# Optimization experiments

Hardware: AMD Instinct MI355X
Metric: run time of the kernel (lower is better)

The kernel has to match this reference:

```python
import jax, jax.numpy as jnp
import numpy as np

DIN = 1024
DOUT = 1024


def setup_inputs() -> dict:
    key = jax.random.key(0)
    kx, kq, kk, kv = jax.random.split(key, 4)
    B, T = 4, 2048
    x = jax.random.normal(kx, (B, T, DIN), dtype=jnp.float32)
    # nn.Linear weights are (dout, din); init like PyTorch default scale
    s = 1.0 / np.sqrt(DIN)
    Wq = jax.random.uniform(kq, (DOUT, DIN), minval=-s, maxval=s, dtype=jnp.float32)
    Wk = jax.random.uniform(kk, (DOUT, DIN), minval=-s, maxval=s, dtype=jnp.float32)
    Wv = jax.random.uniform(kv, (DOUT, DIN), minval=-s, maxval=s, dtype=jnp.float32)
    return {"x": x, "Wq": Wq, "Wk": Wk, "Wv": Wv}


def reference(x, Wq, Wk, Wv):
    B, T, _ = x.shape
    q = jnp.einsum('btd,ed->bte', x, Wq)
    k = jnp.einsum('btd,ed->bte', x, Wk)
    v = jnp.einsum('btd,ed->bte', x, Wv)
    attn = jnp.einsum('bqe,bke->bqk', q, k)  # [B, T, T]
    # Faithful to source: masked_fill result is discarded, so the causal mask
    # is a MULTIPLICATIVE tril of ones (upper triangle logits become 0, not -inf).
    mask = jnp.tril(jnp.ones((T, T), dtype=attn.dtype))
    attn = attn * mask
    # Faithful to source: scale by sqrt(last dim of attn) = sqrt(T), not sqrt(d).
    attn = jax.nn.softmax(attn / jnp.sqrt(jnp.asarray(T, attn.dtype)), axis=-1)
    return jnp.einsum('bqk,bke->bqe', attn, v)
```

## Files before the change

### kernel.cpp

```cpp
#include <hip/hip_runtime.h>
#include <stdint.h>

#define BB 4
#define TT 2048
#define DD 1024
#define NX (BB*TT*DD)
#define NW (DD*DD)
#define SCALE 0.022097086912079608f
#define SCALEI 2.157918643757774e-5f
#define UNSCALE 7.689469810104304e-6f
#define Q8F 2.4606299212598425e-4f
#define VQ 48.0f
#define PVF (1.0f/3072.0f)
#define TQF (1.0f/24.0f)

typedef short v8s __attribute__((ext_vector_type(8)));
typedef float v4f __attribute__((ext_vector_type(4)));
typedef int   v4i __attribute__((ext_vector_type(4)));
typedef uint8_t u8;

typedef const void __attribute__((address_space(1))) *as1_cvp;
typedef void __attribute__((address_space(3))) *as3_vp;

__device__ __forceinline__ short f2bf(float f) {
    union { float f; uint32_t u; } x; x.f = f;
    uint32_t r = x.u + 0x7fffu + ((x.u >> 16) & 1u);
    return (short)(r >> 16);
}

__device__ __forceinline__ void gl_lds16(const void* g, const void* lds_wave_base) {
    __builtin_amdgcn_global_load_lds(
        (as1_cvp)(uintptr_t)g,
        (as3_vp)(uint32_t)(uintptr_t)lds_wave_base,
        16, 0, 0);
}

#define WAITV(N) asm volatile("s_waitcnt vmcnt(" #N ")" ::: "memory")

__device__ __forceinline__ void stage128B(const u8* __restrict__ g, int lda,
                                          u8* lds, int tid) {
    #pragma unroll
    for (int s = 0; s < 2; s++) {
        int t = s * 512 + tid;
        int r = t >> 3, c = t & 7, cg = c ^ (r & 7);
        gl_lds16(g + (size_t)r * lda + cg * 16, lds + s * 8192 + (tid >> 6) * 1024);
    }
}
__device__ __forceinline__ void stB8(const u8* __restrict__ g, u8* lds, int tid, int p) {
    #pragma unroll
    for (int s = 0; s < 2; s++) {
        int t = s * 512 + tid;
        int r = t >> 3, c = t & 7, cg = c ^ (r & 7);
        int grow = ((r >> 5) << 6) + p * 32 + (r & 31);
        gl_lds16(g + (size_t)grow * 1024 + cg * 16, lds + s * 8192 + (tid >> 6) * 1024);
    }
}
__device__ __forceinline__ v4i frag16(const u8* lds, int row, int c) {
    return *(const v4i*)(lds + row * 128 + ((c ^ (row & 7)) << 4));
}

__device__ __forceinline__ void stage64(const u8* __restrict__ g, u8* lds, int tid) {
    int r = tid >> 2, c = tid & 3;
    gl_lds16(g + (size_t)r * 1024 + c * 16, lds + (tid >> 6) * 1024);
}
__device__ __forceinline__ v4i fragK64(const u8* lds, int row, int gq) {
    return *(const v4i*)(lds + row * 64 + gq * 16);
}

__global__ void k_convert(const float* __restrict__ x, const float* __restrict__ Wq,
                          const float* __restrict__ Wk, const float* __restrict__ Wv,
                          u8* __restrict__ dst8, float* __restrict__ rowsum,
                          float* __restrict__ TSpart, int* __restrict__ TQint) {
    int i = blockIdx.x * 256 + threadIdx.x;
    if (i < BB * TT) rowsum[i] = (float)((15 - ((i & 2047) >> 7)) * 128);
    if (i < BB * 16 * 1024) { TSpart[i] = 0.f; TQint[i] = 0; }
    size_t base = (size_t)i * 4;
    const float* src; size_t off; float sc; bool clip;
    if (base < NX)               { src = x;  off = base; sc = 32.f; clip = true; }
    else if (base < NX + NW)     { src = Wq; off = base - NX; sc = 4064.f; clip = false; }
    else if (base < NX + 2*(size_t)NW) { src = Wk; off = base - NX - NW; sc = 4064.f; clip = false; }
    else                         { src = Wv; off = base - NX - 2*(size_t)NW; sc = 4064.f; clip = false; }
    float4 f = *(const float4*)(src + off);
    float a0 = f.x * sc, a1 = f.y * sc, a2 = f.z * sc, a3 = f.w * sc;
    if (clip) {
        a0 = fminf(fmaxf(a0, -127.f), 127.f);
        a1 = fminf(fmaxf(a1, -127.f), 127.f);
        a2 = fminf(fmaxf(a2, -127.f), 127.f);
        a3 = fminf(fmaxf(a3, -127.f), 127.f);
    }
    int q0 = __float2int_rn(a0), q1 = __float2int_rn(a1);
    int q2 = __float2int_rn(a2), q3 = __float2int_rn(a3);
    uint32_t w = (uint32_t)(q0 & 255) | ((uint32_t)(q1 & 255) << 8) |
                 ((uint32_t)(q2 & 255) << 16) | ((uint32_t)(q3 & 255) << 24);
    *(uint32_t*)(dst8 + base) = w;
}

__global__ __launch_bounds__(512, 2) void k_qkv(const u8* __restrict__ xb,
                                                const u8* __restrict__ wb,
                                                u8* __restrict__ q8,
                                                u8* __restrict__ k8,
                                                u8* __restrict__ vt8,
                                                float* __restrict__ TSpart,
                                                int* __restrict__ TQint) {
    int h = blockIdx.x;
    int w = (h & 7) * 96 + (h >> 3);
    int which = w >> 8, rem = w & 255, ntile = rem >> 6, mtile = rem & 63;
    int m0 = mtile * 128, n0 = ntile * 256;
    const u8* Ag = xb + (size_t)m0 * 1024;
    const u8* Bg = wb + (size_t)which * NW + (size_t)n0 * 1024;
    __shared__ __align__(16) u8 SH[98304];
    int tid = threadIdx.x, lane = tid & 63, wave = tid >> 6;
    int wm = wave >> 2, wn = wave & 3;
    int lr = lane & 15, lq = lane >> 4;
    int arow = wm * 64 + lr;
    int brow = wn * 32 + lr;
    v4i acc[4][4];
    #pragma unroll
    for (int i = 0; i < 4; i++)
        #pragma unroll
        for (int j = 0; j < 4; j++) acc[i][j] = (v4i){0, 0, 0, 0};

    stage128B(Ag, 1024, SH, tid);
    stB8(Bg, SH + 16384, tid, 0);
    stB8(Bg, SH + 32768, tid, 1);

    #pragma unroll
    for (int t = 0; t < 8; ++t) {
        u8* S  = SH + (t & 1) * 49152;
        u8* Sn = SH + ((t + 1) & 1) * 49152;
        const u8* Agn = Ag + (t + 1) * 128;
        const u8* Bgn = Bg + (t + 1) * 128;
        WAITV(2);
        __builtin_amdgcn_s_barrier();
        v4i af[4][2], bf[2][2];
        #pragma unroll
        for (int i = 0; i < 4; i++)
            #pragma unroll
            for (int kh = 0; kh < 2; kh++) af[i][kh] = frag16(S, arow + i * 16, kh * 4 + lq);
        #pragma unroll
        for (int jj = 0; jj < 2; jj++)
            #pragma unroll
            for (int kh = 0; kh < 2; kh++) bf[jj][kh] = frag16(S + 16384, brow + jj * 16, kh * 4 + lq);
        if (t < 7) {
            stage128B(Agn, 1024, Sn,  tid);
            stB8(Bgn, Sn + 16384, tid, 0);
        }
        __builtin_amdgcn_s_setprio(1);
        #pragma unroll
        for (int kh = 0; kh < 2; kh++)
            #pragma unroll
            for (int i = 0; i < 4; i++)
                #pragma unroll
                for (int jj = 0; jj < 2; jj++)
                    acc[i][jj] = __builtin_amdgcn_mfma_i32_16x16x64_i8(af[i][kh], bf[jj][kh], acc[i][jj], 0, 0, 0);
        __builtin_amdgcn_s_setprio(0);
        if (t < 7) { WAITV(4); }
        else       { WAITV(0); }
        __builtin_amdgcn_s_barrier();
        v4i bg2[2][2];
        #pragma unroll
        for (int jj = 0; jj < 2; jj++)
            #pragma unroll
            for (int kh = 0; kh < 2; kh++) bg2[jj][kh] = frag16(S + 32768, brow + jj * 16, kh * 4 + lq);
        if (t < 7) stB8(Bgn, Sn + 32768, tid, 1);
        __builtin_amdgcn_s_setprio(1);
        #pragma unroll
        for (int kh = 0; kh < 2; kh++)
            #pragma unroll
            for (int i = 0; i < 4; i++)
                #pragma unroll
                for (int jj = 0; jj < 2; jj++)
                    acc[i][2 + jj] = __builtin_amdgcn_mfma_i32_16x16x64_i8(af[i][kh], bg2[jj][kh], acc[i][2 + jj], 0, 0, 0);
        __builtin_amdgcn_s_setprio(0);
    }

    if (which == 2) {
        int bb = m0 >> 11, jt = (m0 & 2047) >> 7;
        #pragma unroll
        for (int bI = 0; bI < 4; bI++) {
            int col = n0 + wn * 64 + bI * 16 + lr;
            float sf = 0.f; int si = 0;
            #pragma unroll
            for (int a = 0; a < 4; a++) {
                int row0 = m0 + wm * 64 + a * 16 + lq * 4;
                int tt0 = row0 & 2047;
                size_t idx = ((size_t)bb << 21) + ((size_t)col << 11) + tt0;
                float v0 = (float)acc[a][bI][0] * UNSCALE;
                float v1 = (float)acc[a][bI][1] * UNSCALE;
                float v2 = (float)acc[a][bI][2] * UNSCALE;
                float v3 = (float)acc[a][bI][3] * UNSCALE;
                sf += v0 + v1 + v2 + v3;
                int c0 = __float2int_rn(fminf(fmaxf(v0 * VQ, -127.f), 127.f));
                int c1 = __float2int_rn(fminf(fmaxf(v1 * VQ, -127.f), 127.f));
                int c2 = __float2int_rn(fminf(fmaxf(v2 * VQ, -127.f), 127.f));
                int c3 = __float2int_rn(fminf(fmaxf(v3 * VQ, -127.f), 127.f));
                si += c0 + c1 + c2 + c3;
                uint32_t pw = (uint32_t)(c0 & 255) | ((uint32_t)(c1 & 255) << 8) |
                              ((uint32_t)(c2 & 255) << 16) | ((uint32_t)(c3 & 255) << 24);
                *(uint32_t*)(vt8 + idx) = pw;
            }
            sf += __shfl_xor(sf, 16); sf += __shfl_xor(sf, 32);
            si += __shfl_xor(si, 16); si += __shfl_xor(si, 32);
            if (lq == 0) {
                atomicAdd(&TSpart[(size_t)(bb * 16 + jt) * 1024 + col], sf);
                atomicAdd(&TQint[(size_t)(bb * 16 + jt) * 1024 + col], si);
            }
        }
    } else {
        u8* outp = (which == 0) ? q8 : k8;
        #pragma unroll
        for (int a = 0; a < 4; a++)
            #pragma unroll
            for (int b = 0; b < 4; b++)
                #pragma unroll
                for (int r = 0; r < 4; r++) {
                    int row = m0 + wm * 64 + a * 16 + lq * 4 + r;
                    int col = n0 + wn * 64 + b * 16 + lr;
                    float v = (float)acc[a][b][r] * Q8F;
                    v = fminf(fmaxf(v, -127.f), 127.f);
                    outp[(size_t)row * 1024 + col] = (u8)(__float2int_rn(v) & 255);
                }
    }
}

__global__ __launch_bounds__(512, 4) void k_pk(const u8* __restrict__ q8,
                                               const u8* __restrict__ k8,
                                               char* __restrict__ P8,
                                               float* __restrict__ rowsum) {
    int pidx = blockIdx.x, b = blockIdx.z;
    int qt = 0;
    while ((qt + 1) * (qt + 2) / 2 <= pidx) qt++;
    int kt = pidx - qt * (qt + 1) / 2;
    int r0 = qt * 128;
    const u8* Ag = q8 + ((size_t)b * 2048 + r0) * 1024;
    const u8* Bg = k8 + ((size_t)b * 2048 + (size_t)kt * 128) * 1024;
    __shared__ __align__(16) u8 SH[49152];
    int tid = threadIdx.x, lane = tid & 63, wave = tid >> 6;
    int wm2 = wave >> 2, wn4 = wave & 3;
    int lr = lane & 15, lq = lane >> 4;
    v4i acc[4][2];
    #pragma unroll
    for (int i = 0; i < 4; i++)
        #pragma unroll
        for (int j = 0; j < 2; j++) acc[i][j] = (v4i){0, 0, 0, 0};

    stage64(Ag,      SH,                tid);
    stage64(Bg,      SH + 8192,         tid);
    stage64(Ag + 64, SH + 16384,        tid);
    stage64(Bg + 64, SH + 16384 + 8192, tid);

    #pragma unroll
    for (int it = 0; it < 16; ++it) {
        if (it + 1 < 16) { WAITV(2); }
        else             { WAITV(0); }
        __builtin_amdgcn_s_barrier();
        if (it + 2 < 16) {
            u8* Sn = SH + ((it + 2) % 3) * 16384;
            stage64(Ag + (it + 2) * 64, Sn,        tid);
            stage64(Bg + (it + 2) * 64, Sn + 8192, tid);
        }
        const u8* S = SH + (it % 3) * 16384;
        v4i af[4], bf[2];
        #pragma unroll
        for (int i = 0; i < 4; i++) af[i] = fragK64(S, wm2 * 64 + i * 16 + lr, lq);
        #pragma unroll
        for (int j = 0; j < 2; j++) bf[j] = fragK64(S + 8192, wn4 * 32 + j * 16 + lr, lq);
        __builtin_amdgcn_s_setprio(1);
        #pragma unroll
        for (int i = 0; i < 4; i++)
            #pragma unroll
            for (int j = 0; j < 2; j++)
                acc[i][j] = __builtin_amdgcn_mfma_i32_16x16x64_i8(af[i], bf[j], acc[i][j], 0, 0, 0);
        __builtin_amdgcn_s_setprio(0);
    }
    char* Pb = P8 + ((size_t)b << 22);
    float rs[4][4];
    #pragma unroll
    for (int i = 0; i < 4; i++)
        #pragma unroll
        for (int r = 0; r < 4; r++) rs[i][r] = 0.f;
    #pragma unroll
    for (int i = 0; i < 4; i++)
        #pragma unroll
        for (int j = 0; j < 2; j++)
            #pragma unroll
            for (int r = 0; r < 4; r++) {
                int qi = r0 + wm2 * 64 + i * 16 + lq * 4 + r;
                int kj = kt * 128 + wn4 * 32 + j * 16 + lr;
                float p = (kj <= qi) ? __expf((float)acc[i][j][r] * SCALEI) : 1.0f;
                int u = __float2int_rn(fminf(p * 64.f, 255.f));
                Pb[(size_t)qi * 2048 + kj] = (char)(u - 128);
                rs[i][r] += (float)u * 0.015625f;
            }
    #pragma unroll
    for (int m = 1; m < 16; m <<= 1)
        #pragma unroll
        for (int i = 0; i < 4; i++)
            #pragma unroll
            for (int r = 0; r < 4; r++) rs[i][r] += __shfl_xor(rs[i][r], m);
    if (lr == 0)
        #pragma unroll
        for (int i = 0; i < 4; i++)
            #pragma unroll
            for (int r = 0; r < 4; r++)
                atomicAdd(&rowsum[b * 2048 + r0 + wm2 * 64 + i * 16 + lq * 4 + r], rs[i][r]);
}

__global__ __launch_bounds__(512, 2) void k_pv(const u8* __restrict__ P8,
                                               const u8* __restrict__ vt8,
                                               const float* __restrict__ rowsum,
                                               const float* __restrict__ TSpart,
                                               const int* __restrict__ TQint,
                                               float* __restrict__ out) {
    int et = blockIdx.x, p = blockIdx.y, b = blockIdx.z;
    const u8* Bg = vt8 + ((size_t)b << 21) + (size_t)et * 128 * 2048;
    __shared__ __align__(16) u8 SH[98304];
    __shared__ float tsq[128], tqq[128];
    int tid = threadIdx.x, lane = tid & 63, wave = tid >> 6;
    int wm2 = wave >> 2, wn4 = wave & 3;
    int lr = lane & 15, lq = lane >> 4;

    #pragma unroll
    for (int ph = 0; ph < 2; ph++) {
        int qt = ph ? p : 15 - p;
        int r0 = qt * 128;
        int iters = qt + 1;
        const u8* Ag = P8 + ((size_t)b << 22) + (size_t)r0 * 2048;
        v4i acc[4][2];
        #pragma unroll
        for (int i = 0; i < 4; i++)
            #pragma unroll
            for (int j = 0; j < 2; j++) acc[i][j] = (v4i){0, 0, 0, 0};

        stage128B(Ag, 2048, SH,         tid);
        stage128B(Bg, 2048, SH + 16384, tid);
        if (iters > 1) {
            stage128B(Ag + 128, 2048, SH + 32768,         tid);
            stage128B(Bg + 128, 2048, SH + 32768 + 16384, tid);
        }
        if (tid < 128) {
            int e = et * 128 + tid;
            float ts = 0.f;
            for (int jt = qt + 1; jt < 16; jt++) ts += TSpart[(size_t)(b * 16 + jt) * 1024 + e];
            int tq = 0;
            for (int jt = 0; jt <= qt; jt++) tq += TQint[(size_t)(b * 16 + jt) * 1024 + e];
            tsq[tid] = ts;
            tqq[tid] = (float)tq;
            asm volatile("s_waitcnt lgkmcnt(0)" ::: "memory");
        }

        for (int it = 0; it < iters; ++it) {
            if (it + 1 < iters) { WAITV(4); }
            else                { WAITV(0); }
            __builtin_amdgcn_s_barrier();
            if (it + 2 < iters) {
                u8* Sn = SH + ((it + 2) % 3) * 32768;
                stage128B(Ag + (it + 2) * 128, 2048, Sn,         tid);
                stage128B(Bg + (it + 2) * 128, 2048, Sn + 16384, tid);
            }
            const u8* S = SH + (it % 3) * 32768;
            v4i af[4][2], bf[2][2];
            #pragma unroll
            for (int i = 0; i < 4; i++)
                #pragma unroll
                for (int kh = 0; kh < 2; kh++) af[i][kh] = frag16(S, wm2 * 64 + i * 16 + lr, kh * 4 + lq);
            #pragma unroll
            for (int j = 0; j < 2; j++)
                #pragma unroll
                for (int kh = 0; kh < 2; kh++) bf[j][kh] = frag16(S + 16384, wn4 * 32 + j * 16 + lr, kh * 4 + lq);
            __builtin_amdgcn_s_setprio(1);
            #pragma unroll
            for (int kh = 0; kh < 2; kh++)
                #pragma unroll
                for (int i = 0; i < 4; i++)
                    #pragma unroll
                    for (int j = 0; j < 2; j++)
                        acc[i][j] = __builtin_amdgcn_mfma_i32_16x16x64_i8(af[i][kh], bf[j][kh], acc[i][j], 0, 0, 0);
            __builtin_amdgcn_s_setprio(0);
        }
        #pragma unroll
        for (int i = 0; i < 4; i++)
            #pragma unroll
            for (int j = 0; j < 2; j++)
                #pragma unroll
                for (int r = 0; r < 4; r++) {
                    int row = r0 + wm2 * 64 + i * 16 + lq * 4 + r;
                    int cl = wn4 * 32 + j * 16 + lr;
                    int col = et * 128 + cl;
                    float numer = (float)acc[i][j][r] * PVF + tqq[cl] * TQF + tsq[cl];
                    out[((size_t)(b * 2048 + row) << 10) + col] = numer / rowsum[b * 2048 + row];
                }
        __builtin_amdgcn_s_barrier();
    }
}

extern "C" void kernel_launch(void* const* d_in, const int* in_sizes, int n_in,
                              void* d_out, int out_size, void* d_ws, size_t ws_size,
                              hipStream_t stream) {
    const float* x  = (const float*)d_in[0];
    const float* Wq = (const float*)d_in[1];
    const float* Wk = (const float*)d_in[2];
    const float* Wv = (const float*)d_in[3];
    float* out = (float*)d_out;
    char* ws = (char*)d_ws;

    u8*    xb8    = (u8*)(ws + 0);
    u8*    q8     = (u8*)(ws + 11534336);
    u8*    k8     = (u8*)(ws + 19922944);
    u8*    vt8    = (u8*)(ws + 28311552);
    char*  P8     = (char*)(ws + 36700160);
    float* rowsum = (float*)(ws + 53477376);
    float* TSpart = (float*)(ws + 53510144);
    int*   TQint  = (int*)(ws + 53772288);

    k_convert<<<11264, 256, 0, stream>>>(x, Wq, Wk, Wv, xb8, rowsum, TSpart, TQint);
    k_qkv<<<dim3(768, 1, 1), 512, 0, stream>>>(xb8, xb8 + NX, q8, k8, vt8, TSpart, TQint);
    k_pk<<<dim3(136, 1, 4), 512, 0, stream>>>(q8, k8, P8, rowsum);
    k_pv<<<dim3(8, 8, 4), 512, 0, stream>>>((const u8*)P8, vt8, rowsum, TSpart, TQint, out);
}
```

Before: 190.6 us.

## Double the M tile of the int8 QKV GEMM to 256 rows per block

The QKV projection kernel now computes a 256x256 output tile per block instead of 128x256, halving the grid to 384 blocks. Each wave holds 8x4 accumulators and loads A fragments inside the k-half loop, so every B fragment feeds twice as many MFMAs. LDS grows to 128KB with double buffering, and the wait counts and V-statistics tile indices are adjusted. The aim is to reduce redundant B loads and LDS traffic per MFMA, at the cost of higher register and LDS pressure and lower occupancy (launch bounds still request 2 blocks per CU, which 128KB of LDS may not allow).

```diff
diff --git a/kernel.cpp b/kernel.cpp
--- a/kernel.cpp
+++ b/kernel.cpp
@@ -44,6 +44,14 @@
         int t = s * 512 + tid;
         int r = t >> 3, c = t & 7, cg = c ^ (r & 7);
         gl_lds16(g + (size_t)r * lda + cg * 16, lds + s * 8192 + (tid >> 6) * 1024);
+    }
+}
+__device__ __forceinline__ void stA256(const u8* __restrict__ g, u8* lds, int tid) {
+    #pragma unroll
+    for (int s = 0; s < 4; s++) {
+        int t = s * 512 + tid;
+        int r = t >> 3, c = t & 7, cg = c ^ (r & 7);
+        gl_lds16(g + (size_t)r * 1024 + cg * 16, lds + s * 8192 + (tid >> 6) * 1024);
     }
 }
 __device__ __forceinline__ void stB8(const u8* __restrict__ g, u8* lds, int tid, int p) {
@@ -103,86 +111,90 @@
                                                 float* __restrict__ TSpart,
                                                 int* __restrict__ TQint) {
     int h = blockIdx.x;
-    int w = (h & 7) * 96 + (h >> 3);
-    int which = w >> 8, rem = w & 255, ntile = rem >> 6, mtile = rem & 63;
-    int m0 = mtile * 128, n0 = ntile * 256;
+    int w = (h & 7) * 48 + (h >> 3);
+    int which = w >> 7, rem = w & 127, ntile = rem >> 5, mtile = rem & 31;
+    int m0 = mtile * 256, n0 = ntile * 256;
     const u8* Ag = xb + (size_t)m0 * 1024;
     const u8* Bg = wb + (size_t)which * NW + (size_t)n0 * 1024;
-    __shared__ __align__(16) u8 SH[98304];
+    __shared__ __align__(16) u8 SH[131072];
     int tid = threadIdx.x, lane = tid & 63, wave = tid >> 6;
     int wm = wave >> 2, wn = wave & 3;
     int lr = lane & 15, lq = lane >> 4;
-    int arow = wm * 64 + lr;
+    int arow = wm * 128 + lr;
     int brow = wn * 32 + lr;
-    v4i acc[4][4];
-    #pragma unroll
-    for (int i = 0; i < 4; i++)
+    v4i acc[8][4];
+    #pragma unroll
+    for (int i = 0; i < 8; i++)
         #pragma unroll
         for (int j = 0; j < 4; j++) acc[i][j] = (v4i){0, 0, 0, 0};
 
-    stage128B(Ag, 1024, SH, tid);
-    stB8(Bg, SH + 16384, tid, 0);
-    stB8(Bg, SH + 32768, tid, 1);
+    stA256(Ag, SH, tid);
+    stB8(Bg, SH + 32768, tid, 0);
+    stB8(Bg, SH + 49152, tid, 1);
 
     #pragma unroll
     for (int t = 0; t < 8; ++t) {
-        u8* S  = SH + (t & 1) * 49152;
-        u8* Sn = SH + ((t + 1) & 1) * 49152;
+        u8* S  = SH + (t & 1) * 65536;
+        u8* Sn = SH + ((t + 1) & 1) * 65536;
         const u8* Agn = Ag + (t + 1) * 128;
         const u8* Bgn = Bg + (t + 1) * 128;
         WAITV(2);
         __builtin_amdgcn_s_barrier();
-        v4i af[4][2], bf[2][2];
-        #pragma unroll
-        for (int i = 0; i < 4; i++)
-            #pragma unroll
-            for (int kh = 0; kh < 2; kh++) af[i][kh] = frag16(S, arow + i * 16, kh * 4 + lq);
-        #pragma unroll
-        for (int jj = 0; jj < 2; jj++)
-            #pragma unroll
-            for (int kh = 0; kh < 2; kh++) bf[jj][kh] = frag16(S + 16384, brow + jj * 16, kh * 4 + lq);
+        v4i bf[2][2];
+        #pragma unroll
+        for (int j = 0; j < 2; j++)
+            #pragma unroll
+            for (int kh = 0; kh < 2; kh++) bf[j][kh] = frag16(S + 32768, brow + j * 16, kh * 4 + lq);
         if (t < 7) {
-            stage128B(Agn, 1024, Sn,  tid);
-            stB8(Bgn, Sn + 16384, tid, 0);
+            stA256(Agn, Sn, tid);
+            stB8(Bgn, Sn + 32768, tid, 0);
         }
         __builtin_amdgcn_s_setprio(1);
         #pragma unroll
-        for (int kh = 0; kh < 2; kh++)
-            #pragma unroll
-            for (int i = 0; i < 4; i++)
-                #pragma unroll
-                for (int jj = 0; jj < 2; jj++)
-                    acc[i][jj] = __builtin_amdgcn_mfma_i32_16x16x64_i8(af[i][kh], bf[jj][kh], acc[i][jj], 0, 0, 0);
+        for (int kh = 0; kh < 2; kh++) {
+            v4i af[8];
+            #pragma unroll
+            for (int i = 0; i < 8; i++) af[i] = frag16(S, arow + i * 16, kh * 4 + lq);
+            #pragma unroll
+            for (int i = 0; i < 8; i++)
+                #pragma unroll
+                for (int j = 0; j < 2; j++)
+                    acc[i][j] = __builtin_amdgcn_mfma_i32_16x16x64_i8(af[i], bf[j][kh], acc[i][j], 0, 0, 0);
+        }
         __builtin_amdgcn_s_setprio(0);
-        if (t < 7) { WAITV(4); }
+        if (t < 7) { WAITV(6); }
         else       { WAITV(0); }
         __builtin_amdgcn_s_barrier();
-        v4i bg2[2][2];
-        #pragma unroll
-        for (int jj = 0; jj < 2; jj++)
-            #pragma unroll
-            for (int kh = 0; kh < 2; kh++) bg2[jj][kh] = frag16(S + 32768, brow + jj * 16, kh * 4 + lq);
-        if (t < 7) stB8(Bgn, Sn + 32768, tid, 1);
+        #pragma unroll
+        for (int j = 0; j < 2; j++)
+            #pragma unroll
+            for (int kh = 0; kh < 2; kh++) bf[j][kh] = frag16(S + 49152, brow + j * 16, kh * 4 + lq);
+        if (t < 7) stB8(Bgn, Sn + 49152, tid, 1);
         __builtin_amdgcn_s_setprio(1);
         #pragma unroll
-        for (int kh = 0; kh < 2; kh++)
-            #pragma unroll
-            for (int i = 0; i < 4; i++)
-                #pragma unroll
-                for (int jj = 0; jj < 2; jj++)
-                    acc[i][2 + jj] = __builtin_amdgcn_mfma_i32_16x16x64_i8(af[i][kh], bg2[jj][kh], acc[i][2 + jj], 0, 0, 0);
+        for (int kh = 0; kh < 2; kh++) {
+            v4i af[8];
+            #pragma unroll
+            for (int i = 0; i < 8; i++) af[i] = frag16(S, arow + i * 16, kh * 4 + lq);
+            #pragma unroll
+            for (int i = 0; i < 8; i++)
+                #pragma unroll
+                for (int j = 0; j < 2; j++)
+                    acc[i][2 + j] = __builtin_amdgcn_mfma_i32_16x16x64_i8(af[i], bf[j][kh], acc[i][2 + j], 0, 0, 0);
+        }
         __builtin_amdgcn_s_setprio(0);
     }
 
     if (which == 2) {
-        int bb = m0 >> 11, jt = (m0 & 2047) >> 7;
+        int bb = m0 >> 11;
+        int jt = ((m0 & 2047) >> 7) + wm;
         #pragma unroll
         for (int bI = 0; bI < 4; bI++) {
             int col = n0 + wn * 64 + bI * 16 + lr;
             float sf = 0.f; int si = 0;
             #pragma unroll
-            for (int a = 0; a < 4; a++) {
-                int row0 = m0 + wm * 64 + a * 16 + lq * 4;
+            for (int a = 0; a < 8; a++) {
+                int row0 = m0 + wm * 128 + a * 16 + lq * 4;
                 int tt0 = row0 & 2047;
                 size_t idx = ((size_t)bb << 21) + ((size_t)col << 11) + tt0;
                 float v0 = (float)acc[a][bI][0] * UNSCALE;
@@ -209,12 +221,12 @@
     } else {
         u8* outp = (which == 0) ? q8 : k8;
         #pragma unroll
-        for (int a = 0; a < 4; a++)
+        for (int a = 0; a < 8; a++)
             #pragma unroll
             for (int b = 0; b < 4; b++)
                 #pragma unroll
                 for (int r = 0; r < 4; r++) {
-                    int row = m0 + wm * 64 + a * 16 + lq * 4 + r;
+                    int row = m0 + wm * 128 + a * 16 + lq * 4 + r;
                     int col = n0 + wn * 64 + b * 16 + lr;
                     float v = (float)acc[a][b][r] * Q8F;
                     v = fminf(fmaxf(v, -127.f), 127.f);
@@ -414,7 +426,7 @@
     int*   TQint  = (int*)(ws + 53772288);
 
     k_convert<<<11264, 256, 0, stream>>>(x, Wq, Wk, Wv, xb8, rowsum, TSpart, TQint);
-    k_qkv<<<dim3(768, 1, 1), 512, 0, stream>>>(xb8, xb8 + NX, q8, k8, vt8, TSpart, TQint);
+    k_qkv<<<dim3(384, 1, 1), 512, 0, stream>>>(xb8, xb8 + NX, q8, k8, vt8, TSpart, TQint);
     k_pk<<<dim3(136, 1, 4), 512, 0, stream>>>(q8, k8, P8, rowsum);
     k_pv<<<dim3(8, 8, 4), 512, 0, stream>>>((const u8*)P8, vt8, rowsum, TSpart, TQint, out);
 }
```

After: 194.1 us. No clear change (+1.8%).

## Triple-buffer QKV and PK GEMM pipelines with 128-byte K steps

Applied to the files above, without the earlier changes.

The QKV GEMM moves from a double-buffered loop, where the B tile was staged in two interleaved halves with two barriers per step, to a triple-buffered loop. Each step now stages the full 256-row B tile in one go and uses a single barrier, at the cost of 144 KB of LDS per block. The PK kernel moves from 64-byte K steps with a 3-stage ring to 128-byte K steps with a 3-stage ring. That halves the iteration and barrier count, but raises LDS to 96 KB and lowers launch bounds from 4 to 2 blocks. The aim is to hide more global-load latency and cut synchronisation overhead, with the risk of lower occupancy per CU.

```diff
diff --git a/kernel.cpp b/kernel.cpp
--- a/kernel.cpp
+++ b/kernel.cpp
@@ -14,19 +14,12 @@
 #define PVF (1.0f/3072.0f)
 #define TQF (1.0f/24.0f)
 
-typedef short v8s __attribute__((ext_vector_type(8)));
 typedef float v4f __attribute__((ext_vector_type(4)));
 typedef int   v4i __attribute__((ext_vector_type(4)));
 typedef uint8_t u8;
 
 typedef const void __attribute__((address_space(1))) *as1_cvp;
 typedef void __attribute__((address_space(3))) *as3_vp;
-
-__device__ __forceinline__ short f2bf(float f) {
-    union { float f; uint32_t u; } x; x.f = f;
-    uint32_t r = x.u + 0x7fffu + ((x.u >> 16) & 1u);
-    return (short)(r >> 16);
-}
 
 __device__ __forceinline__ void gl_lds16(const void* g, const void* lds_wave_base) {
     __builtin_amdgcn_global_load_lds(
@@ -46,25 +39,16 @@
         gl_lds16(g + (size_t)r * lda + cg * 16, lds + s * 8192 + (tid >> 6) * 1024);
     }
 }
-__device__ __forceinline__ void stB8(const u8* __restrict__ g, u8* lds, int tid, int p) {
-    #pragma unroll
-    for (int s = 0; s < 2; s++) {
+__device__ __forceinline__ void stage256B(const u8* __restrict__ g, u8* lds, int tid) {
+    #pragma unroll
+    for (int s = 0; s < 4; s++) {
         int t = s * 512 + tid;
         int r = t >> 3, c = t & 7, cg = c ^ (r & 7);
-        int grow = ((r >> 5) << 6) + p * 32 + (r & 31);
-        gl_lds16(g + (size_t)grow * 1024 + cg * 16, lds + s * 8192 + (tid >> 6) * 1024);
+        gl_lds16(g + (size_t)r * 1024 + cg * 16, lds + s * 8192 + (tid >> 6) * 1024);
     }
 }
 __device__ __forceinline__ v4i frag16(const u8* lds, int row, int c) {
     return *(const v4i*)(lds + row * 128 + ((c ^ (row & 7)) << 4));
-}
-
-__device__ __forceinline__ void stage64(const u8* __restrict__ g, u8* lds, int tid) {
-    int r = tid >> 2, c = tid & 3;
-    gl_lds16(g + (size_t)r * 1024 + c * 16, lds + (tid >> 6) * 1024);
-}
-__device__ __forceinline__ v4i fragK64(const u8* lds, int row, int gq) {
-    return *(const v4i*)(lds + row * 64 + gq * 16);
 }
 
 __global__ void k_convert(const float* __restrict__ x, const float* __restrict__ Wq,
@@ -108,69 +92,51 @@
     int m0 = mtile * 128, n0 = ntile * 256;
     const u8* Ag = xb + (size_t)m0 * 1024;
     const u8* Bg = wb + (size_t)which * NW + (size_t)n0 * 1024;
-    __shared__ __align__(16) u8 SH[98304];
+    __shared__ __align__(16) u8 SH[147456];
     int tid = threadIdx.x, lane = tid & 63, wave = tid >> 6;
     int wm = wave >> 2, wn = wave & 3;
     int lr = lane & 15, lq = lane >> 4;
     int arow = wm * 64 + lr;
-    int brow = wn * 32 + lr;
+    int brow = wn * 64 + lr;
     v4i acc[4][4];
     #pragma unroll
     for (int i = 0; i < 4; i++)
         #pragma unroll
         for (int j = 0; j < 4; j++) acc[i][j] = (v4i){0, 0, 0, 0};
 
-    stage128B(Ag, 1024, SH, tid);
-    stB8(Bg, SH + 16384, tid, 0);
-    stB8(Bg, SH + 32768, tid, 1);
+    stage128B(Ag,       1024, SH,                 tid);
+    stage256B(Bg,             SH + 16384,         tid);
+    stage128B(Ag + 128, 1024, SH + 49152,         tid);
+    stage256B(Bg + 128,       SH + 49152 + 16384, tid);
 
     #pragma unroll
     for (int t = 0; t < 8; ++t) {
-        u8* S  = SH + (t & 1) * 49152;
-        u8* Sn = SH + ((t + 1) & 1) * 49152;
-        const u8* Agn = Ag + (t + 1) * 128;
-        const u8* Bgn = Bg + (t + 1) * 128;
-        WAITV(2);
+        if (t + 1 < 8) { WAITV(6); }
+        else           { WAITV(0); }
         __builtin_amdgcn_s_barrier();
-        v4i af[4][2], bf[2][2];
+        if (t + 2 < 8) {
+            u8* Sn = SH + ((t + 2) % 3) * 49152;
+            stage128B(Ag + (t + 2) * 128, 1024, Sn,         tid);
+            stage256B(Bg + (t + 2) * 128,       Sn + 16384, tid);
+        }
+        const u8* S = SH + (t % 3) * 49152;
+        v4i af[4][2], bf[4][2];
         #pragma unroll
         for (int i = 0; i < 4; i++)
             #pragma unroll
             for (int kh = 0; kh < 2; kh++) af[i][kh] = frag16(S, arow + i * 16, kh * 4 + lq);
         #pragma unroll
-        for (int jj = 0; jj < 2; jj++)
-            #pragma unroll
-            for (int kh = 0; kh < 2; kh++) bf[jj][kh] = frag16(S + 16384, brow + jj * 16, kh * 4 + lq);
-        if (t < 7) {
-            stage128B(Agn, 1024, Sn,  tid);
-            stB8(Bgn, Sn + 16384, tid, 0);
-        }
+        for (int j = 0; j < 4; j++)
+            #pragma unroll
+            for (int kh = 0; kh < 2; kh++) bf[j][kh] = frag16(S + 16384, brow + j * 16, kh * 4 + lq);
         __builtin_amdgcn_s_setprio(1);
         #pragma unroll
         for (int kh = 0; kh < 2; kh++)
             #pragma unroll
             for (int i = 0; i < 4; i++)
                 #pragma unroll
-                for (int jj = 0; jj < 2; jj++)
-                    acc[i][jj] = __builtin_amdgcn_mfma_i32_16x16x64_i8(af[i][kh], bf[jj][kh], acc[i][jj], 0, 0, 0);
-        __builtin_amdgcn_s_setprio(0);
-        if (t < 7) { WAITV(4); }
-        else       { WAITV(0); }
-        __builtin_amdgcn_s_barrier();
-        v4i bg2[2][2];
-        #pragma unroll
-        for (int jj = 0; jj < 2; jj++)
-            #pragma unroll
-            for (int kh = 0; kh < 2; kh++) bg2[jj][kh] = frag16(S + 32768, brow + jj * 16, kh * 4 + lq);
-        if (t < 7) stB8(Bgn, Sn + 32768, tid, 1);
-        __builtin_amdgcn_s_setprio(1);
-        #pragma unroll
-        for (int kh = 0; kh < 2; kh++)
-            #pragma unroll
-            for (int i = 0; i < 4; i++)
-                #pragma unroll
-                for (int jj = 0; jj < 2; jj++)
-                    acc[i][2 + jj] = __builtin_amdgcn_mfma_i32_16x16x64_i8(af[i][kh], bg2[jj][kh], acc[i][2 + jj], 0, 0, 0);
+                for (int j = 0; j < 4; j++)
+                    acc[i][j] = __builtin_amdgcn_mfma_i32_16x16x64_i8(af[i][kh], bf[j][kh], acc[i][j], 0, 0, 0);
         __builtin_amdgcn_s_setprio(0);
     }
 
@@ -223,7 +189,7 @@
     }
 }
 
-__global__ __launch_bounds__(512, 4) void k_pk(const u8* __restrict__ q8,
+__global__ __launch_bounds__(512, 2) void k_pk(const u8* __restrict__ q8,
                                                const u8* __restrict__ k8,
                                                char* __restrict__ P8,
                                                float* __restrict__ rowsum) {
@@ -234,7 +200,7 @@
     int r0 = qt * 128;
     const u8* Ag = q8 + ((size_t)b * 2048 + r0) * 1024;
     const u8* Bg = k8 + ((size_t)b * 2048 + (size_t)kt * 128) * 1024;
-    __shared__ __align__(16) u8 SH[49152];
+    __shared__ __align__(16) u8 SH[98304];
     int tid = threadIdx.x, lane = tid & 63, wave = tid >> 6;
     int wm2 = wave >> 2, wn4 = wave & 3;
     int lr = lane & 15, lq = lane >> 4;
@@ -244,33 +210,39 @@
         #pragma unroll
         for (int j = 0; j < 2; j++) acc[i][j] = (v4i){0, 0, 0, 0};
 
-    stage64(Ag,      SH,                tid);
-    stage64(Bg,      SH + 8192,         tid);
-    stage64(Ag + 64, SH + 16384,        tid);
-    stage64(Bg + 64, SH + 16384 + 8192, tid);
-
-    #pragma unroll
-    for (int it = 0; it < 16; ++it) {
-        if (it + 1 < 16) { WAITV(2); }
-        else             { WAITV(0); }
+    stage128B(Ag,       1024, SH,                 tid);
+    stage128B(Bg,       1024, SH + 16384,         tid);
+    stage128B(Ag + 128, 1024, SH + 32768,         tid);
+    stage128B(Bg + 128, 1024, SH + 32768 + 16384, tid);
+
+    #pragma unroll
+    for (int it = 0; it < 8; ++it) {
+        if (it + 1 < 8) { WAITV(4); }
+        else            { WAITV(0); }
         __builtin_amdgcn_s_barrier();
-        if (it + 2 < 16) {
-            u8* Sn = SH + ((it + 2) % 3) * 16384;
-            stage64(Ag + (it + 2) * 64, Sn,        tid);
-            stage64(Bg + (it + 2) * 64, Sn + 8192, tid);
-        }
-        const u8* S = SH + (it % 3) * 16384;
-        v4i af[4], bf[2];
-        #pragma unroll
-        for (int i = 0; i < 4; i++) af[i] = fragK64(S, wm2 * 64 + i * 16 + lr, lq);
-        #pragma unroll
-        for (int j = 0; j < 2; j++) bf[j] = fragK64(S + 8192, wn4 * 32 + j * 16 + lr, lq);
+        if (it + 2 < 8) {
+            u8* Sn = SH + ((it + 2) % 3) * 32768;
+            stage128B(Ag + (it + 2) * 128, 1024, Sn,         tid);
+            stage128B(Bg + (it + 2) * 128, 1024, Sn + 16384, tid);
+        }
+        const u8* S = SH + (it % 3) * 32768;
+        v4i af[4][2], bf[2][2];
+        #pragma unroll
+        for (int i = 0; i < 4; i++)
+            #pragma unroll
+            for (int kh = 0; kh < 2; kh++) af[i][kh] = frag16(S, wm2 * 64 + i * 16 + lr, kh * 4 + lq);
+        #pragma unroll
+        for (int j = 0; j < 2; j++)
+            #pragma unroll
+            for (int kh = 0; kh < 2; kh++) bf[j][kh] = frag16(S + 16384, wn4 * 32 + j * 16 + lr, kh * 4 + lq);
         __builtin_amdgcn_s_setprio(1);
         #pragma unroll
-        for (int i = 0; i < 4; i++)
-            #pragma unroll
-            for (int j = 0; j < 2; j++)
-                acc[i][j] = __builtin_amdgcn_mfma_i32_16x16x64_i8(af[i], bf[j], acc[i][j], 0, 0, 0);
+        for (int kh = 0; kh < 2; kh++)
+            #pragma unroll
+            for (int i = 0; i < 4; i++)
+                #pragma unroll
+                for (int j = 0; j < 2; j++)
+                    acc[i][j] = __builtin_amdgcn_mfma_i32_16x16x64_i8(af[i][kh], bf[j][kh], acc[i][j], 0, 0, 0);
         __builtin_amdgcn_s_setprio(0);
     }
     char* Pb = P8 + ((size_t)b << 22);
```

Result: slower. 196.2 us (+2.9%).
